# Performance work log

Measured on AMD Instinct MI355X. Metric: run time of the kernel, lower is better.

## Reference

```python
import jax, jax.numpy as jnp
import numpy as np
import math

B, D, H, W, C = 1, 16, 56, 56, 256
WD, WH, WW = 2, 7, 7
NH, NP = 8, 4
N = WD * WH * WW          # 98 tokens per window
HD = C // NH
NWIN = (D // WD) * (H // WH) * (W // WW)  # 512


def layernorm(x, g, b, eps=1e-5):
    m = x.mean(-1, keepdims=True)
    v = jnp.mean((x - m) ** 2, -1, keepdims=True)
    return (x - m) * jax.lax.rsqrt(v + eps) * g + b


def _reference_points():
    zz = (jnp.arange(WD, dtype=jnp.float32) + 0.5) / WD
    yy = (jnp.arange(WH, dtype=jnp.float32) + 0.5) / WH
    xx = (jnp.arange(WW, dtype=jnp.float32) + 0.5) / WW
    gz, gy, gx = jnp.meshgrid(zz, yy, xx, indexing='ij')
    return jnp.stack([gx.ravel(), gy.ravel(), gz.ravel()], -1)  # (N, 3) in xyz order


def _trilinear(value, loc):
    # value: (Bn, N, NH, HD); loc: (Bn, N, NH, NP, 3) normalized xyz in [0,1]
    # grid_sample semantics: align_corners=False, zero padding
    Bn = value.shape[0]
    v = value.transpose(0, 2, 1, 3)  # (Bn, NH, S, HD), S == N (window volume)
    px = loc[..., 0] * WW - 0.5
    py = loc[..., 1] * WH - 0.5
    pz = loc[..., 2] * WD - 0.5
    x0, y0, z0 = jnp.floor(px), jnp.floor(py), jnp.floor(pz)
    out = jnp.zeros(loc.shape[:-1] + (HD,), value.dtype)
    for dz in (0, 1):
        for dy in (0, 1):
            for dx in (0, 1):
                xi, yi, zi = x0 + dx, y0 + dy, z0 + dz
                wgt = (1 - jnp.abs(px - xi)) * (1 - jnp.abs(py - yi)) * (1 - jnp.abs(pz - zi))
                valid = ((xi >= 0) & (xi < WW) & (yi >= 0) & (yi < WH) & (zi >= 0) & (zi < WD)).astype(value.dtype)
                idx = (jnp.clip(zi, 0, WD - 1) * (WH * WW) + jnp.clip(yi, 0, WH - 1) * WW
                       + jnp.clip(xi, 0, WW - 1)).astype(jnp.int32)  # (Bn, N, NH, NP)
                idxf = idx.transpose(0, 2, 1, 3).reshape(Bn, NH, N * NP)
                g = jnp.take_along_axis(v, idxf[..., None], axis=2)  # (Bn, NH, N*NP, HD)
                g = g.reshape(Bn, NH, N, NP, HD).transpose(0, 2, 1, 3, 4)
                out = out + g * (wgt * valid)[..., None]
    return out  # (Bn, N, NH, NP, HD)


def setup_inputs():
    key = jax.random.key(0)
    ks = jax.random.split(key, 12)

    def lin(k, fin, fout):
        s = 1.0 / np.sqrt(fin)
        kw, kb = jax.random.split(k)
        return (jax.random.uniform(kw, (fin, fout), jnp.float32, -s, s),
                jax.random.uniform(kb, (fout,), jnp.float32, -s, s))

    val_w, val_b = lin(ks[2], C, C)
    off_w, off_b = lin(ks[3], C, NH * NP * 3)
    aw_w, aw_b = lin(ks[4], C, NH * NP)
    out_w, out_b = lin(ks[5], C, C)
    proj_w, proj_b = lin(ks[6], C, C)
    fc1_w, fc1_b = lin(ks[7], C, 4 * C)
    fc2_w, fc2_b = lin(ks[8], 4 * C, C)
    return dict(
        x=jax.random.normal(ks[0], (B, D, H, W, C), jnp.float32),
        mask=jax.random.uniform(ks[1], (NWIN, N, WD, WH, WW), jnp.float32),
        norm1_g=jnp.ones((C,), jnp.float32), norm1_b=jnp.zeros((C,), jnp.float32),
        val_w=val_w, val_b=val_b, off_w=off_w, off_b=off_b,
        aw_w=aw_w, aw_b=aw_b, out_w=out_w, out_b=out_b,
        anorm_g=jnp.ones((C,), jnp.float32), anorm_b=jnp.zeros((C,), jnp.float32),
        proj_w=proj_w, proj_b=proj_b,
        norm2_g=jnp.ones((C,), jnp.float32), norm2_b=jnp.zeros((C,), jnp.float32),
        fc1_w=fc1_w, fc1_b=fc1_b, fc2_w=fc2_w, fc2_b=fc2_b)


def reference(x, mask, norm1_g, norm1_b, val_w, val_b, off_w, off_b, aw_w, aw_b,
              out_w, out_b, anorm_g, anorm_b, proj_w, proj_b,
              norm2_g, norm2_b, fc1_w, fc1_b, fc2_w, fc2_b):
    shortcut = x
    xn = layernorm(x, norm1_g, norm1_b)
    # window partition (dims divisible by window, shift_size = 0 -> no pad/roll)
    xw = xn.reshape(B, D // WD, WD, H // WH, WH, W // WW, WW, C)
    xw = xw.transpose(0, 1, 3, 5, 2, 4, 6, 7).reshape(-1, N, C)  # (B*NWIN, N, C)
    Bn = B * NWIN
    # --- PositionEmbeddingSine over the per-window mask ---
    z_e = jnp.cumsum(mask, 2) * mask / math.pi
    y_e = jnp.cumsum(mask, 3) * mask / math.pi
    x_e = jnp.cumsum(mask, 4) * mask / math.pi
    emb = mask * (jnp.sin(x_e) + jnp.sin(math.pi * y_e) + z_e)
    emb = emb.reshape(NWIN, N, N)  # flatten(2); N == WD*WH*WW
    diag = jnp.diagonal(emb, axis1=1, axis2=2)  # (NWIN, N)
    q = (xw.reshape(B, NWIN, N, C) + diag[None, :, :, None]).reshape(Bn, N, C)
    # --- MS3DDeformAttn over single level = window ---
    ref = _reference_points()  # (N, 3)
    value = (xw @ val_w + val_b).reshape(Bn, N, NH, HD)
    off = (q @ off_w + off_b).reshape(Bn, N, NH, NP, 3)
    aw = jax.nn.softmax((q @ aw_w + aw_b).reshape(Bn, N, NH, NP), axis=-1)
    loc = ref[None, :, None, None, :] + off / jnp.array([WW, WH, WD], jnp.float32)
    sampled = _trilinear(value, loc)                       # (Bn, N, NH, NP, HD)
    attn = (sampled * aw[..., None]).sum(3).reshape(Bn, N, C) @ out_w + out_b
    # WindowAttention3D epilogue: proj(norm(x + attn))
    xw = layernorm(xw + attn, anorm_g, anorm_b) @ proj_w + proj_b
    # window reverse
    xr = xw.reshape(B, D // WD, H // WH, W // WW, WD, WH, WW, C)
    xr = xr.transpose(0, 1, 4, 2, 5, 3, 6, 7).reshape(B, D, H, W, C)
    x = shortcut + xr
    # MLP branch
    h = layernorm(x, norm2_g, norm2_b)
    h = jax.nn.gelu(h @ fc1_w + fc1_b)
    return x + (h @ fc2_w + fc2_b)
```

## Files before the change

### kernel.cpp

```cpp
#include <hip/hip_runtime.h>
#include <hip/hip_bf16.h>
#include <hip/hip_fp16.h>

#define B2F(x) __bfloat162float(x)
#define F2B(x) __float2bfloat16(x)

typedef __bf16 bf16x8 __attribute__((ext_vector_type(8)));
typedef float floatx4 __attribute__((ext_vector_type(4)));

static constexpr int MROWS = 50176;
static constexpr int CDIM  = 256;
static constexpr int MCHUNK = 25088;

enum { MODE_BF16 = 0, MODE_VALOFFAW = 1, MODE_REVERSE = 3, MODE_GELU = 4, MODE_FC2 = 5 };

#if defined(__has_builtin)
#if __has_builtin(__builtin_amdgcn_global_load_lds)
#define HAS_GLL 1
#endif
#endif
#ifndef HAS_GLL
#define HAS_GLL 0
#endif


__device__ __forceinline__ void win_decode(int r, int& tok) {
    int w = r / 98, n = r - w * 98;
    int dB = w >> 6, hB = (w >> 3) & 7, wB = w & 7;
    int z = n / 49, n2 = n - z * 49, yy = n2 / 7, xx = n2 - yy * 7;
    tok = ((dB * 2 + z) * 56 + hB * 7 + yy) * 56 + wB * 7 + xx;
}

__device__ __forceinline__ float bf2f(unsigned short u) {
    return __uint_as_float(((unsigned)u) << 16);
}

__device__ __forceinline__ float wave_sum64(float v) {
#pragma unroll
    for (int off = 32; off > 0; off >>= 1) v += __shfl_xor(v, off, 64);
    return v;
}


__global__ __launch_bounds__(256) void transpose_all(
    const float* __restrict__ val_w, const float* __restrict__ off_w,
    const float* __restrict__ aw_w,  const float* __restrict__ out_w,
    const float* __restrict__ proj_w, const float* __restrict__ fc1_w,
    const float* __restrict__ fc2_w,
    __hip_bfloat16* __restrict__ valT, __hip_bfloat16* __restrict__ offawT,
    __hip_bfloat16* __restrict__ outT, __hip_bfloat16* __restrict__ projT,
    __hip_bfloat16* __restrict__ fc1T, __hip_bfloat16* __restrict__ fc2T) {
    int bid = blockIdx.x;
    const float* src; __hip_bfloat16* dst; int K, N, base;
    if (bid < 256)       { src = val_w;  dst = valT;           K = 256;  N = 256;  base = 0; }
    else if (bid < 352)  { src = off_w;  dst = offawT;         K = 256;  N = 96;   base = 256; }
    else if (bid < 384)  { src = aw_w;   dst = offawT + 96*256; K = 256; N = 32;   base = 352; }
    else if (bid < 640)  { src = out_w;  dst = outT;           K = 256;  N = 256;  base = 384; }
    else if (bid < 896)  { src = proj_w; dst = projT;          K = 256;  N = 256;  base = 640; }
    else if (bid < 1920) { src = fc1_w;  dst = fc1T;           K = 256;  N = 1024; base = 896; }
    else                 { src = fc2_w;  dst = fc2T;           K = 1024; N = 256;  base = 1920; }
    int i = (bid - base) * 256 + threadIdx.x;
    if (i >= K * N) return;
    int nn = i / K, kk = i - nn * K;
    dst[(size_t)nn * K + kk] = F2B(src[(size_t)kk * N + nn]);
}


__global__ __launch_bounds__(256) void diag_colsum_kernel(
    const float* __restrict__ mask, float* __restrict__ diag,
    const __hip_bfloat16* __restrict__ wT, float* __restrict__ csum) {
    if (blockIdx.x == gridDim.x - 1) {
        int n = threadIdx.x;
        if (n < 128) {
            float s = 0.f;
            for (int k = 0; k < 256; ++k) s += B2F(wT[n * 256 + k]);
            csum[n] = s;
        }
        return;
    }
    int r = blockIdx.x * 256 + threadIdx.x;
    int n = r % 98;
    int z = n / 49, n2 = n - z * 49, yy = n2 / 7, xx = n2 - yy * 7;
    const float* mb = mask + (size_t)r * 98;
    float m = mb[z * 49 + yy * 7 + xx];
    float sz = 0.f, sy = 0.f, sx = 0.f;
    for (int k = 0; k <= z; ++k)  sz += mb[k * 49 + yy * 7 + xx];
    for (int k = 0; k <= yy; ++k) sy += mb[z * 49 + k * 7 + xx];
    for (int k = 0; k <= xx; ++k) sx += mb[z * 49 + yy * 7 + k];
    const float PI = 3.14159265358979323846f;
    diag[r] = m * (sinf(sx * m / PI) + sinf(sy * m) + sz * m / PI);
}


__global__ __launch_bounds__(256) void ln1_kernel(
    const float* __restrict__ x,
    const float* __restrict__ g, const float* __restrict__ b,
    __hip_bfloat16* __restrict__ xw) {
    const int lane = threadIdx.x & 63;
    const int r = blockIdx.x * 4 + (threadIdx.x >> 6);
    int tok; win_decode(r, tok);
    const int c0 = lane * 4;
    float4 v = *(const float4*)(x + (size_t)tok * CDIM + c0);
    float mean = wave_sum64(v.x + v.y + v.z + v.w) * (1.f / 256.f);
    float dx = v.x - mean, dy = v.y - mean, dz = v.z - mean, dw = v.w - mean;
    float var = wave_sum64(dx * dx + dy * dy + dz * dz + dw * dw) * (1.f / 256.f);
    float rstd = rsqrtf(var + 1e-5f);
    float4 gg = *(const float4*)(g + c0);
    float4 bb = *(const float4*)(b + c0);
    __hip_bfloat16 ob[4] = { F2B(dx * rstd * gg.x + bb.x), F2B(dy * rstd * gg.y + bb.y),
                             F2B(dz * rstd * gg.z + bb.z), F2B(dw * rstd * gg.w + bb.w) };
    *(ushort4*)(xw + (size_t)r * CDIM + c0) = *(const ushort4*)ob;
}

__global__ __launch_bounds__(256) void ln_a_kernel(
    const __hip_bfloat16* __restrict__ xw, const __hip_bfloat16* __restrict__ attn,
    const float* __restrict__ g, const float* __restrict__ b,
    __hip_bfloat16* a2) {
    const int lane = threadIdx.x & 63;
    const int r = blockIdx.x * 4 + (threadIdx.x >> 6);
    const int c0 = lane * 4;
    const size_t base = (size_t)r * CDIM + c0;
    ushort4 xv = *(const ushort4*)(xw + base);
    ushort4 av = *(const ushort4*)(attn + base);
    float tx = bf2f(xv.x) + bf2f(av.x);
    float ty = bf2f(xv.y) + bf2f(av.y);
    float tz = bf2f(xv.z) + bf2f(av.z);
    float tw = bf2f(xv.w) + bf2f(av.w);
    float mean = wave_sum64(tx + ty + tz + tw) * (1.f / 256.f);
    float dx = tx - mean, dy = ty - mean, dz = tz - mean, dw = tw - mean;
    float var = wave_sum64(dx * dx + dy * dy + dz * dz + dw * dw) * (1.f / 256.f);
    float rstd = rsqrtf(var + 1e-5f);
    float4 gg = *(const float4*)(g + c0);
    float4 bb = *(const float4*)(b + c0);
    __hip_bfloat16 ob[4] = { F2B(dx * rstd * gg.x + bb.x), F2B(dy * rstd * gg.y + bb.y),
                             F2B(dz * rstd * gg.z + bb.z), F2B(dw * rstd * gg.w + bb.w) };
    *(ushort4*)((__hip_bfloat16*)a2 + base) = *(const ushort4*)ob;
}

__global__ __launch_bounds__(256) void ln2_kernel(
    const float* __restrict__ xres,
    const float* __restrict__ g, const float* __restrict__ b,
    __hip_bfloat16* __restrict__ hin) {
    const int lane = threadIdx.x & 63;
    const int r = blockIdx.x * 4 + (threadIdx.x >> 6);
    const int c0 = lane * 4;
    float4 v = *(const float4*)(xres + (size_t)r * CDIM + c0);
    float mean = wave_sum64(v.x + v.y + v.z + v.w) * (1.f / 256.f);
    float dx = v.x - mean, dy = v.y - mean, dz = v.z - mean, dw = v.w - mean;
    float var = wave_sum64(dx * dx + dy * dy + dz * dz + dw * dw) * (1.f / 256.f);
    float rstd = rsqrtf(var + 1e-5f);
    float4 gg = *(const float4*)(g + c0);
    float4 bb = *(const float4*)(b + c0);
    __hip_bfloat16 ob[4] = { F2B(dx * rstd * gg.x + bb.x), F2B(dy * rstd * gg.y + bb.y),
                             F2B(dz * rstd * gg.z + bb.z), F2B(dw * rstd * gg.w + bb.w) };
    *(ushort4*)(hin + (size_t)r * CDIM + c0) = *(const ushort4*)ob;
}


__global__ __launch_bounds__(512, 6) void sample_fused(
    const __half* __restrict__ offaw,
    const __hip_bfloat16* __restrict__ value,
    __hip_bfloat16* __restrict__ ai) {
    __shared__ __align__(16) __hip_bfloat16 vs[98 * 256];
    const int tid = threadIdx.x;
    const int w = blockIdx.x;

    {
        const uint4* vsrc = (const uint4*)(value + (size_t)w * 98 * CDIM);
        uint4* vdst = (uint4*)vs;
        for (int i = tid; i < 98 * CDIM / 8; i += 512) vdst[i] = vsrc[i];
    }
    __syncthreads();

    const int lane  = tid & 63;
    const int wave  = tid >> 6;
    const int h     = lane >> 3;
    const int s     = lane & 7;
    const int p     = s >> 1;
    const int jbase = (s & 1) * 4;
    const int c0    = lane * 4;
    const int gbase = lane & ~7;

    for (int r = wave; r < 98; r += 8) {
        int z = r / 49, n2 = r - z * 49, yy = n2 / 7, xx = n2 - yy * 7;
        const __half* orow = offaw + ((size_t)w * 98 + r) * 128;

        float l0 = __half2float(orow[96 + h * 4 + 0]);
        float l1 = __half2float(orow[96 + h * 4 + 1]);
        float l2 = __half2float(orow[96 + h * 4 + 2]);
        float l3 = __half2float(orow[96 + h * 4 + 3]);
        float mx = fmaxf(fmaxf(l0, l1), fmaxf(l2, l3));
        float e0 = __expf(l0 - mx), e1 = __expf(l1 - mx), e2 = __expf(l2 - mx), e3 = __expf(l3 - mx);
        float inv = 1.f / (e0 + e1 + e2 + e3);
        float ep = (p == 0) ? e0 : (p == 1) ? e1 : (p == 2) ? e2 : e3;
        float wp = ep * inv;

        float ox = __half2float(orow[h * 12 + p * 3 + 0]);
        float oy = __half2float(orow[h * 12 + p * 3 + 1]);
        float oz = __half2float(orow[h * 12 + p * 3 + 2]);
        float px = (float)xx + ox, py = (float)yy + oy, pz = (float)z + oz;
        float fx0 = floorf(px), fy0 = floorf(py), fz0 = floorf(pz);
        int ix = (int)fx0, iy = (int)fy0, iz = (int)fz0;
        float fx = px - fx0, fy = py - fy0, fz = pz - fz0;

        uint packed[4];
#pragma unroll
        for (int jj = 0; jj < 4; ++jj) {
            int j = jbase + jj;
            int dzz = j >> 2, dyy = (j >> 1) & 1, dxx = j & 1;
            int zi = iz + dzz, yi = iy + dyy, xi = ix + dxx;
            float wz = dzz ? fz : 1.f - fz;
            float wy = dyy ? fy : 1.f - fy;
            float wxw = dxx ? fx : 1.f - fx;
            bool valid = (zi >= 0) & (zi < 2) & (yi >= 0) & (yi < 7) & (xi >= 0) & (xi < 7);
            float wc = valid ? wp * wz * wy * wxw : 0.f;
            int zc = min(max(zi, 0), 1), yc = min(max(yi, 0), 6), xc = min(max(xi, 0), 6);
            int idx = zc * 49 + yc * 7 + xc;
            packed[jj] = ((uint)idx << 16) | (uint)__half_as_ushort(__float2half(wc));
        }

        float a0 = 0.f, a1 = 0.f, a2 = 0.f, a3 = 0.f;
#pragma unroll
        for (int jj = 0; jj < 4; ++jj) {
            uint mine = packed[jj];
#pragma unroll
            for (int sl = 0; sl < 8; ++sl) {
                uint pk = __shfl(mine, gbase + sl, 64);
                float wj = __half2float(__ushort_as_half((unsigned short)(pk & 0xffffu)));
                int idx = (int)(pk >> 16);
                ushort4 v = *(const ushort4*)(vs + (size_t)idx * CDIM + c0);
                a0 += wj * bf2f(v.x);
                a1 += wj * bf2f(v.y);
                a2 += wj * bf2f(v.z);
                a3 += wj * bf2f(v.w);
            }
        }
        __hip_bfloat16 ob[4] = { F2B(a0), F2B(a1), F2B(a2), F2B(a3) };
        *(ushort4*)(ai + ((size_t)w * 98 + r) * CDIM + c0) = *(const ushort4*)ob;
    }
}


template <int MODE>
__global__ __launch_bounds__(256) void gemm_bt(
    const __hip_bfloat16* __restrict__ A,
    const __hip_bfloat16* __restrict__ Bt,
    const int N, const int K,
    const float* __restrict__ bias0,
    const float* __restrict__ bias1,
    const float* __restrict__ bias2,
    void* C,
    void* extra,
    const void* extra2,
    const float* __restrict__ csum) {
    __shared__ __align__(16) __hip_bfloat16 As[2][128 * 32];
    __shared__ __align__(16) __hip_bfloat16 Bs[2][128 * 32];
    const int tid  = threadIdx.x;
    const int lane = tid & 63;
    const int wave = tid >> 6;
    const int wm = (wave >> 1) * 64;
    const int wn = (wave & 1) * 64;
    const int row0 = blockIdx.x * 128;
    const int col0 = blockIdx.y * 128;
    const int l15 = lane & 15;
    const int quad = lane >> 4;

    floatx4 acc[4][4] = {};

    const int sr = tid >> 2;
    const int sk = (tid & 3) * 8;

    const __hip_bfloat16* Ab = A + (size_t)row0 * K + sr * (size_t)K + sk;
    const __hip_bfloat16* Bb = Bt + (size_t)col0 * K + sr * (size_t)K + sk;
    const size_t half64 = (size_t)64 * K;

    auto stage = [&](int buf, int k0) {
#if HAS_GLL
        __builtin_amdgcn_global_load_lds(
            (const __attribute__((address_space(1))) void*)(Ab + k0),
            (__attribute__((address_space(3))) void*)(&As[buf][sr * 32 + sk]), 16, 0, 0);
        __builtin_amdgcn_global_load_lds(
            (const __attribute__((address_space(1))) void*)(Ab + half64 + k0),
            (__attribute__((address_space(3))) void*)(&As[buf][(sr + 64) * 32 + sk]), 16, 0, 0);
        __builtin_amdgcn_global_load_lds(
            (const __attribute__((address_space(1))) void*)(Bb + k0),
            (__attribute__((address_space(3))) void*)(&Bs[buf][sr * 32 + sk]), 16, 0, 0);
        __builtin_amdgcn_global_load_lds(
            (const __attribute__((address_space(1))) void*)(Bb + half64 + k0),
            (__attribute__((address_space(3))) void*)(&Bs[buf][(sr + 64) * 32 + sk]), 16, 0, 0);
#else
        *reinterpret_cast<uint4*>(&As[buf][sr * 32 + sk]) = *reinterpret_cast<const uint4*>(Ab + k0);
        *reinterpret_cast<uint4*>(&As[buf][(sr + 64) * 32 + sk]) = *reinterpret_cast<const uint4*>(Ab + half64 + k0);
        *reinterpret_cast<uint4*>(&Bs[buf][sr * 32 + sk]) = *reinterpret_cast<const uint4*>(Bb + k0);
        *reinterpret_cast<uint4*>(&Bs[buf][(sr + 64) * 32 + sk]) = *reinterpret_cast<const uint4*>(Bb + half64 + k0);
#endif
    };

    const int nk = K >> 5;
    stage(0, 0);
    for (int t = 0; t < nk; ++t) {
        __syncthreads();
        if (t + 1 < nk) stage((t + 1) & 1, (t + 1) * 32);
        const __hip_bfloat16* Asb = As[t & 1];
        const __hip_bfloat16* Bsb = Bs[t & 1];
        bf16x8 af[4], bfg[4];
#pragma unroll
        for (int i = 0; i < 4; ++i)
            af[i] = *reinterpret_cast<const bf16x8*>(&Asb[(wm + i * 16 + l15) * 32 + quad * 8]);
#pragma unroll
        for (int j = 0; j < 4; ++j)
            bfg[j] = *reinterpret_cast<const bf16x8*>(&Bsb[(wn + j * 16 + l15) * 32 + quad * 8]);
#pragma unroll
        for (int i = 0; i < 4; ++i)
#pragma unroll
            for (int j = 0; j < 4; ++j)
                acc[i][j] = __builtin_amdgcn_mfma_f32_16x16x32_bf16(af[i], bfg[j], acc[i][j], 0, 0, 0);
    }

#pragma unroll
    for (int i = 0; i < 4; ++i) {
#pragma unroll
        for (int j = 0; j < 4; ++j) {
#pragma unroll
            for (int rr = 0; rr < 4; ++rr) {
                int row = row0 + wm + i * 16 + quad * 4 + rr;
                int col = col0 + wn + j * 16 + l15;
                float v = acc[i][j][rr];
                if constexpr (MODE == MODE_BF16) {
                    v += bias0[col];
                    ((__hip_bfloat16*)C)[(size_t)row * N + col] = F2B(v);
                } else if constexpr (MODE == MODE_VALOFFAW) {
                    if (col < 256) {
                        v += bias0[col];
                        ((__hip_bfloat16*)C)[(size_t)row * 256 + col] = F2B(v);
                    } else {
                        int c2 = col - 256;
                        const float* diag = (const float*)extra2;
                        v += (c2 < 96 ? bias1[c2] : bias2[c2 - 96]);
                        v += diag[row] * csum[c2];
                        ((__half*)extra)[(size_t)row * 128 + c2] = __float2half(v);
                    }
                } else if constexpr (MODE == MODE_REVERSE) {
                    v += bias0[col];
                    int tok; win_decode(row, tok);
                    const float* xin = (const float*)extra2;
                    ((float*)C)[(size_t)tok * CDIM + col] = xin[(size_t)tok * CDIM + col] + v;
                } else if constexpr (MODE == MODE_GELU) {
                    v += bias0[col];
                    float t2 = 1.5957691216057308f * (v + 0.044715f * v * v * v);
                    v = v / (1.f + __expf(-t2));
                    ((__hip_bfloat16*)C)[(size_t)row * N + col] = F2B(v);
                } else {
                    v += bias0[col];
                    const float* xres = (const float*)extra2;
                    v += xres[(size_t)row * CDIM + col];
                    ((float*)C)[(size_t)row * CDIM + col] = v;
                }
            }
        }
    }
}


extern "C" void kernel_launch(void* const* d_in, const int* in_sizes, int n_in,
                              void* d_out, int out_size, void* d_ws, size_t ws_size,
                              hipStream_t stream) {
    const float* x      = (const float*)d_in[0];
    const float* mask   = (const float*)d_in[1];
    const float* n1g    = (const float*)d_in[2];
    const float* n1b    = (const float*)d_in[3];
    const float* val_w  = (const float*)d_in[4];
    const float* val_b  = (const float*)d_in[5];
    const float* off_w  = (const float*)d_in[6];
    const float* off_b  = (const float*)d_in[7];
    const float* aw_w   = (const float*)d_in[8];
    const float* aw_b   = (const float*)d_in[9];
    const float* out_w  = (const float*)d_in[10];
    const float* out_b  = (const float*)d_in[11];
    const float* ang    = (const float*)d_in[12];
    const float* anb    = (const float*)d_in[13];
    const float* proj_w = (const float*)d_in[14];
    const float* proj_b = (const float*)d_in[15];
    const float* n2g    = (const float*)d_in[16];
    const float* n2b    = (const float*)d_in[17];
    const float* fc1_w  = (const float*)d_in[18];
    const float* fc1_b  = (const float*)d_in[19];
    const float* fc2_w  = (const float*)d_in[20];
    const float* fc2_b  = (const float*)d_in[21];

    char* ws = (char*)d_ws;
    size_t o = 0;
    auto alloc = [&](size_t bytes) {
        size_t r = o;
        o += (bytes + 255) & ~(size_t)255;
        return r;
    };
    const size_t M = MROWS;
    const size_t REGION_B = M * 128 * 2 + M * 256 * 2 + M * 256 * 2;

    __hip_bfloat16* valT    = (__hip_bfloat16*)(ws + alloc(256 * 256 * 2));
    __hip_bfloat16* offawT  = (__hip_bfloat16*)(ws + alloc(128 * 256 * 2));
    __hip_bfloat16* outT    = (__hip_bfloat16*)(ws + alloc(256 * 256 * 2));
    __hip_bfloat16* projT   = (__hip_bfloat16*)(ws + alloc(256 * 256 * 2));
    __hip_bfloat16* fc1T    = (__hip_bfloat16*)(ws + alloc(1024 * 256 * 2));
    __hip_bfloat16* fc2T    = (__hip_bfloat16*)(ws + alloc(256 * 1024 * 2));
    float*          csum    = (float*)(ws + alloc(128 * 4));
    float*          diag    = (float*)(ws + alloc(M * 4));
    char*           slab1   = ws + alloc(M * 256 * 2);
    char*           region  = ws + alloc(REGION_B);
    (void)ws_size; (void)in_sizes; (void)n_in; (void)out_size;

    __hip_bfloat16* xw    = (__hip_bfloat16*)slab1;
    __hip_bfloat16* a2    = (__hip_bfloat16*)slab1;
    __hip_bfloat16* hin   = (__hip_bfloat16*)slab1;
    __half*         offaw = (__half*)region;
    __hip_bfloat16* ai    = (__hip_bfloat16*)(region + M * 128 * 2);
    __hip_bfloat16* hbuf  = (__hip_bfloat16*)region;
    __hip_bfloat16* value = (__hip_bfloat16*)d_out;
    __hip_bfloat16* attn  = (__hip_bfloat16*)d_out;
    float*          xres  = (float*)d_out;

    dim3 blk(256);
    hipLaunchKernelGGL(transpose_all, dim3(2944), blk, 0, stream,
                       val_w, off_w, aw_w, out_w, proj_w, fc1_w, fc2_w,
                       valT, offawT, outT, projT, fc1T, fc2T);
    hipLaunchKernelGGL(diag_colsum_kernel, dim3(MROWS / 256 + 1), blk, 0, stream,
                       mask, diag, offawT, csum);

    hipLaunchKernelGGL(ln1_kernel, dim3(MROWS / 4), blk, 0, stream, x, n1g, n1b, xw);
    hipLaunchKernelGGL((gemm_bt<MODE_VALOFFAW>), dim3(MROWS / 128, 3), blk, 0, stream,
                       xw, valT, 384, 256, val_b, off_b, aw_b,
                       (void*)value, (void*)offaw, (const void*)diag, csum);
    hipLaunchKernelGGL(sample_fused, dim3(MROWS / 98), dim3(512), 0, stream,
                       offaw, value, ai);
    hipLaunchKernelGGL((gemm_bt<MODE_BF16>), dim3(MROWS / 128, 2), blk, 0, stream,
                       ai, outT, 256, 256, out_b, (const float*)nullptr, (const float*)nullptr,
                       (void*)attn, (void*)nullptr, (const void*)nullptr, (const float*)nullptr);
    hipLaunchKernelGGL(ln_a_kernel, dim3(MROWS / 4), blk, 0, stream, xw, attn, ang, anb, a2);
    hipLaunchKernelGGL((gemm_bt<MODE_REVERSE>), dim3(MROWS / 128, 2), blk, 0, stream,
                       a2, projT, 256, 256, proj_b, (const float*)nullptr, (const float*)nullptr,
                       (void*)xres, (void*)nullptr, (const void*)x, (const float*)nullptr);
    hipLaunchKernelGGL(ln2_kernel, dim3(MROWS / 4), blk, 0, stream, xres, n2g, n2b, hin);
    for (int c = 0; c < 2; ++c) {
        const __hip_bfloat16* hin_c = hin + (size_t)c * MCHUNK * 256;
        float*                out_c = (float*)d_out + (size_t)c * MCHUNK * 256;
        hipLaunchKernelGGL((gemm_bt<MODE_GELU>), dim3(MCHUNK / 128, 8), blk, 0, stream,
                           hin_c, fc1T, 1024, 256, fc1_b, (const float*)nullptr, (const float*)nullptr,
                           (void*)hbuf, (void*)nullptr, (const void*)nullptr, (const float*)nullptr);
        hipLaunchKernelGGL((gemm_bt<MODE_FC2>), dim3(MCHUNK / 128, 2), blk, 0, stream,
                           hbuf, fc2T, 256, 1024, fc2_b, (const float*)nullptr, (const float*)nullptr,
                           (void*)out_c, (void*)nullptr, (const void*)out_c, (const float*)nullptr);
    }
}
```

Before: 514.5 us.

## Fuse prologue kernels, stage offsets in LDS, fold residual into out-proj GEMM

Merges the weight transpose, diag/colsum and LN1 kernels into one launch, and computes the column sums from the fp32 weights. The sampling kernel now stages the offset/attention rows in LDS alongside the values, using global_load_lds when available, and packs byte offsets so the inner gather skips an index multiply. The out-proj GEMM adds the xw residual in its epilogue, so the LN kernel reads one tensor instead of two. The MLP runs as a single chunk when the workspace is large enough. The trade-off is extra LDS per block, which lowers the occupancy hint for the sampling kernel.

```diff
diff --git a/kernel.cpp b/kernel.cpp
--- a/kernel.cpp
+++ b/kernel.cpp
@@ -12,7 +12,7 @@
 static constexpr int CDIM  = 256;
 static constexpr int MCHUNK = 25088;
 
-enum { MODE_BF16 = 0, MODE_VALOFFAW = 1, MODE_REVERSE = 3, MODE_GELU = 4, MODE_FC2 = 5 };
+enum { MODE_BF16 = 0, MODE_VALOFFAW = 1, MODE_REVERSE = 3, MODE_GELU = 4, MODE_FC2 = 5, MODE_ATTN = 6 };
 
 #if defined(__has_builtin)
 #if __has_builtin(__builtin_amdgcn_global_load_lds)
@@ -42,7 +42,10 @@
 }
 
 
-__global__ __launch_bounds__(256) void transpose_all(
+__global__ __launch_bounds__(256) void fused_pre(
+    const float* __restrict__ x, const float* __restrict__ n1g, const float* __restrict__ n1b,
+    __hip_bfloat16* __restrict__ xw,
+    const float* __restrict__ mask, float* __restrict__ diag, float* __restrict__ csum,
     const float* __restrict__ val_w, const float* __restrict__ off_w,
     const float* __restrict__ aw_w,  const float* __restrict__ out_w,
     const float* __restrict__ proj_w, const float* __restrict__ fc1_w,
@@ -50,82 +53,74 @@
     __hip_bfloat16* __restrict__ valT, __hip_bfloat16* __restrict__ offawT,
     __hip_bfloat16* __restrict__ outT, __hip_bfloat16* __restrict__ projT,
     __hip_bfloat16* __restrict__ fc1T, __hip_bfloat16* __restrict__ fc2T) {
-    int bid = blockIdx.x;
-    const float* src; __hip_bfloat16* dst; int K, N, base;
-    if (bid < 256)       { src = val_w;  dst = valT;           K = 256;  N = 256;  base = 0; }
-    else if (bid < 352)  { src = off_w;  dst = offawT;         K = 256;  N = 96;   base = 256; }
-    else if (bid < 384)  { src = aw_w;   dst = offawT + 96*256; K = 256; N = 32;   base = 352; }
-    else if (bid < 640)  { src = out_w;  dst = outT;           K = 256;  N = 256;  base = 384; }
-    else if (bid < 896)  { src = proj_w; dst = projT;          K = 256;  N = 256;  base = 640; }
-    else if (bid < 1920) { src = fc1_w;  dst = fc1T;           K = 256;  N = 1024; base = 896; }
-    else                 { src = fc2_w;  dst = fc2T;           K = 1024; N = 256;  base = 1920; }
-    int i = (bid - base) * 256 + threadIdx.x;
-    if (i >= K * N) return;
-    int nn = i / K, kk = i - nn * K;
-    dst[(size_t)nn * K + kk] = F2B(src[(size_t)kk * N + nn]);
-}
-
-
-__global__ __launch_bounds__(256) void diag_colsum_kernel(
-    const float* __restrict__ mask, float* __restrict__ diag,
-    const __hip_bfloat16* __restrict__ wT, float* __restrict__ csum) {
-    if (blockIdx.x == gridDim.x - 1) {
-        int n = threadIdx.x;
-        if (n < 128) {
+    const int bid = blockIdx.x;
+    const int tid = threadIdx.x;
+
+    if (bid < 2944) {
+        const float* src; __hip_bfloat16* dst; int K, N, base;
+        if (bid < 256)       { src = val_w;  dst = valT;            K = 256;  N = 256;  base = 0; }
+        else if (bid < 352)  { src = off_w;  dst = offawT;          K = 256;  N = 96;   base = 256; }
+        else if (bid < 384)  { src = aw_w;   dst = offawT + 96*256; K = 256;  N = 32;   base = 352; }
+        else if (bid < 640)  { src = out_w;  dst = outT;            K = 256;  N = 256;  base = 384; }
+        else if (bid < 896)  { src = proj_w; dst = projT;           K = 256;  N = 256;  base = 640; }
+        else if (bid < 1920) { src = fc1_w;  dst = fc1T;            K = 256;  N = 1024; base = 896; }
+        else                 { src = fc2_w;  dst = fc2T;            K = 1024; N = 256;  base = 1920; }
+        int i = (bid - base) * 256 + tid;
+        if (i >= K * N) return;
+        int nn = i / K, kk = i - nn * K;
+        dst[(size_t)nn * K + kk] = F2B(src[(size_t)kk * N + nn]);
+    } else if (bid < 3140) {
+        int r = (bid - 2944) * 256 + tid;
+        int n = r % 98;
+        int z = n / 49, n2 = n - z * 49, yy = n2 / 7, xx = n2 - yy * 7;
+        const float* mb = mask + (size_t)r * 98;
+        float m = mb[z * 49 + yy * 7 + xx];
+        float sz = 0.f, sy = 0.f, sx = 0.f;
+        for (int k = 0; k <= z; ++k)  sz += mb[k * 49 + yy * 7 + xx];
+        for (int k = 0; k <= yy; ++k) sy += mb[z * 49 + k * 7 + xx];
+        for (int k = 0; k <= xx; ++k) sx += mb[z * 49 + yy * 7 + k];
+        const float PI = 3.14159265358979323846f;
+        diag[r] = m * (sinf(sx * m / PI) + sinf(sy * m) + sz * m / PI);
+    } else if (bid == 3140) {
+        if (tid < 96) {
             float s = 0.f;
-            for (int k = 0; k < 256; ++k) s += B2F(wT[n * 256 + k]);
-            csum[n] = s;
-        }
-        return;
-    }
-    int r = blockIdx.x * 256 + threadIdx.x;
-    int n = r % 98;
-    int z = n / 49, n2 = n - z * 49, yy = n2 / 7, xx = n2 - yy * 7;
-    const float* mb = mask + (size_t)r * 98;
-    float m = mb[z * 49 + yy * 7 + xx];
-    float sz = 0.f, sy = 0.f, sx = 0.f;
-    for (int k = 0; k <= z; ++k)  sz += mb[k * 49 + yy * 7 + xx];
-    for (int k = 0; k <= yy; ++k) sy += mb[z * 49 + k * 7 + xx];
-    for (int k = 0; k <= xx; ++k) sx += mb[z * 49 + yy * 7 + k];
-    const float PI = 3.14159265358979323846f;
-    diag[r] = m * (sinf(sx * m / PI) + sinf(sy * m) + sz * m / PI);
-}
-
-
-__global__ __launch_bounds__(256) void ln1_kernel(
-    const float* __restrict__ x,
-    const float* __restrict__ g, const float* __restrict__ b,
-    __hip_bfloat16* __restrict__ xw) {
-    const int lane = threadIdx.x & 63;
-    const int r = blockIdx.x * 4 + (threadIdx.x >> 6);
-    int tok; win_decode(r, tok);
-    const int c0 = lane * 4;
-    float4 v = *(const float4*)(x + (size_t)tok * CDIM + c0);
-    float mean = wave_sum64(v.x + v.y + v.z + v.w) * (1.f / 256.f);
-    float dx = v.x - mean, dy = v.y - mean, dz = v.z - mean, dw = v.w - mean;
-    float var = wave_sum64(dx * dx + dy * dy + dz * dz + dw * dw) * (1.f / 256.f);
-    float rstd = rsqrtf(var + 1e-5f);
-    float4 gg = *(const float4*)(g + c0);
-    float4 bb = *(const float4*)(b + c0);
-    __hip_bfloat16 ob[4] = { F2B(dx * rstd * gg.x + bb.x), F2B(dy * rstd * gg.y + bb.y),
-                             F2B(dz * rstd * gg.z + bb.z), F2B(dw * rstd * gg.w + bb.w) };
-    *(ushort4*)(xw + (size_t)r * CDIM + c0) = *(const ushort4*)ob;
-}
+            for (int k = 0; k < 256; ++k) s += off_w[(size_t)k * 96 + tid];
+            csum[tid] = s;
+        } else if (tid < 128) {
+            int n = tid - 96;
+            float s = 0.f;
+            for (int k = 0; k < 256; ++k) s += aw_w[(size_t)k * 32 + n];
+            csum[tid] = s;
+        }
+    } else {
+        const int lane = tid & 63;
+        const int r = (bid - 3141) * 4 + (tid >> 6);
+        int tok; win_decode(r, tok);
+        const int c0 = lane * 4;
+        float4 v = *(const float4*)(x + (size_t)tok * CDIM + c0);
+        float mean = wave_sum64(v.x + v.y + v.z + v.w) * (1.f / 256.f);
+        float dx = v.x - mean, dy = v.y - mean, dz = v.z - mean, dw = v.w - mean;
+        float var = wave_sum64(dx * dx + dy * dy + dz * dz + dw * dw) * (1.f / 256.f);
+        float rstd = rsqrtf(var + 1e-5f);
+        float4 gg = *(const float4*)(n1g + c0);
+        float4 bb = *(const float4*)(n1b + c0);
+        __hip_bfloat16 ob[4] = { F2B(dx * rstd * gg.x + bb.x), F2B(dy * rstd * gg.y + bb.y),
+                                 F2B(dz * rstd * gg.z + bb.z), F2B(dw * rstd * gg.w + bb.w) };
+        *(ushort4*)(xw + (size_t)r * CDIM + c0) = *(const ushort4*)ob;
+    }
+}
+
 
 __global__ __launch_bounds__(256) void ln_a_kernel(
-    const __hip_bfloat16* __restrict__ xw, const __hip_bfloat16* __restrict__ attn,
+    const __hip_bfloat16* __restrict__ s,
     const float* __restrict__ g, const float* __restrict__ b,
     __hip_bfloat16* a2) {
     const int lane = threadIdx.x & 63;
     const int r = blockIdx.x * 4 + (threadIdx.x >> 6);
     const int c0 = lane * 4;
     const size_t base = (size_t)r * CDIM + c0;
-    ushort4 xv = *(const ushort4*)(xw + base);
-    ushort4 av = *(const ushort4*)(attn + base);
-    float tx = bf2f(xv.x) + bf2f(av.x);
-    float ty = bf2f(xv.y) + bf2f(av.y);
-    float tz = bf2f(xv.z) + bf2f(av.z);
-    float tw = bf2f(xv.w) + bf2f(av.w);
+    ushort4 sv = *(const ushort4*)(s + base);
+    float tx = bf2f(sv.x), ty = bf2f(sv.y), tz = bf2f(sv.z), tw = bf2f(sv.w);
     float mean = wave_sum64(tx + ty + tz + tw) * (1.f / 256.f);
     float dx = tx - mean, dy = ty - mean, dz = tz - mean, dw = tw - mean;
     float var = wave_sum64(dx * dx + dy * dy + dz * dz + dw * dw) * (1.f / 256.f);
@@ -157,19 +152,46 @@
 }
 
 
-__global__ __launch_bounds__(512, 6) void sample_fused(
+__global__ __launch_bounds__(512, 4) void sample_fused(
     const __half* __restrict__ offaw,
     const __hip_bfloat16* __restrict__ value,
     __hip_bfloat16* __restrict__ ai) {
     __shared__ __align__(16) __hip_bfloat16 vs[98 * 256];
+    __shared__ __align__(16) __half os[98 * 128];
     const int tid = threadIdx.x;
     const int w = blockIdx.x;
 
+#if HAS_GLL
+    {
+        const uint4* vsrc = (const uint4*)(value + (size_t)w * 98 * CDIM);
+#pragma unroll
+        for (int k = 0; k < 7; ++k) {
+            int i = tid + k * 512;
+            if (i < 3136)
+                __builtin_amdgcn_global_load_lds(
+                    (const __attribute__((address_space(1))) void*)(vsrc + i),
+                    (__attribute__((address_space(3))) void*)(((uint4*)vs) + i), 16, 0, 0);
+        }
+        const uint4* osrc = (const uint4*)(offaw + (size_t)w * 98 * 128);
+#pragma unroll
+        for (int k = 0; k < 4; ++k) {
+            int i = tid + k * 512;
+            if (i < 1568)
+                __builtin_amdgcn_global_load_lds(
+                    (const __attribute__((address_space(1))) void*)(osrc + i),
+                    (__attribute__((address_space(3))) void*)(((uint4*)os) + i), 16, 0, 0);
+        }
+    }
+#else
     {
         const uint4* vsrc = (const uint4*)(value + (size_t)w * 98 * CDIM);
         uint4* vdst = (uint4*)vs;
-        for (int i = tid; i < 98 * CDIM / 8; i += 512) vdst[i] = vsrc[i];
-    }
+        for (int i = tid; i < 3136; i += 512) vdst[i] = vsrc[i];
+        const uint4* osrc = (const uint4*)(offaw + (size_t)w * 98 * 128);
+        uint4* odst = (uint4*)os;
+        for (int i = tid; i < 1568; i += 512) odst[i] = osrc[i];
+    }
+#endif
     __syncthreads();
 
     const int lane  = tid & 63;
@@ -178,12 +200,12 @@
     const int s     = lane & 7;
     const int p     = s >> 1;
     const int jbase = (s & 1) * 4;
-    const int c0    = lane * 4;
+    const int boff  = lane * 8;
     const int gbase = lane & ~7;
 
     for (int r = wave; r < 98; r += 8) {
         int z = r / 49, n2 = r - z * 49, yy = n2 / 7, xx = n2 - yy * 7;
-        const __half* orow = offaw + ((size_t)w * 98 + r) * 128;
+        const __half* orow = os + r * 128;
 
         float l0 = __half2float(orow[96 + h * 4 + 0]);
         float l1 = __half2float(orow[96 + h * 4 + 1]);
@@ -216,7 +238,7 @@
             float wc = valid ? wp * wz * wy * wxw : 0.f;
             int zc = min(max(zi, 0), 1), yc = min(max(yi, 0), 6), xc = min(max(xi, 0), 6);
             int idx = zc * 49 + yc * 7 + xc;
-            packed[jj] = ((uint)idx << 16) | (uint)__half_as_ushort(__float2half(wc));
+            packed[jj] = ((uint)(idx * 512) << 16) | (uint)__half_as_ushort(__float2half(wc));
         }
 
         float a0 = 0.f, a1 = 0.f, a2 = 0.f, a3 = 0.f;
@@ -227,8 +249,7 @@
             for (int sl = 0; sl < 8; ++sl) {
                 uint pk = __shfl(mine, gbase + sl, 64);
                 float wj = __half2float(__ushort_as_half((unsigned short)(pk & 0xffffu)));
-                int idx = (int)(pk >> 16);
-                ushort4 v = *(const ushort4*)(vs + (size_t)idx * CDIM + c0);
+                ushort4 v = *(const ushort4*)((const char*)vs + (pk >> 16) + boff);
                 a0 += wj * bf2f(v.x);
                 a1 += wj * bf2f(v.y);
                 a2 += wj * bf2f(v.z);
@@ -236,7 +257,7 @@
             }
         }
         __hip_bfloat16 ob[4] = { F2B(a0), F2B(a1), F2B(a2), F2B(a3) };
-        *(ushort4*)(ai + ((size_t)w * 98 + r) * CDIM + c0) = *(const ushort4*)ob;
+        *(ushort4*)(ai + ((size_t)w * 98 + r) * CDIM + lane * 4) = *(const ushort4*)ob;
     }
 }
 
@@ -328,6 +349,11 @@
                 float v = acc[i][j][rr];
                 if constexpr (MODE == MODE_BF16) {
                     v += bias0[col];
+                    ((__hip_bfloat16*)C)[(size_t)row * N + col] = F2B(v);
+                } else if constexpr (MODE == MODE_ATTN) {
+                    v += bias0[col];
+                    const __hip_bfloat16* xwp = (const __hip_bfloat16*)extra2;
+                    v += B2F(xwp[(size_t)row * 256 + col]);
                     ((__hip_bfloat16*)C)[(size_t)row * N + col] = F2B(v);
                 } else if constexpr (MODE == MODE_VALOFFAW) {
                     if (col < 256) {
@@ -396,7 +422,6 @@
         return r;
     };
     const size_t M = MROWS;
-    const size_t REGION_B = M * 128 * 2 + M * 256 * 2 + M * 256 * 2;
 
     __hip_bfloat16* valT    = (__hip_bfloat16*)(ws + alloc(256 * 256 * 2));
     __hip_bfloat16* offawT  = (__hip_bfloat16*)(ws + alloc(128 * 256 * 2));
@@ -407,8 +432,13 @@
     float*          csum    = (float*)(ws + alloc(128 * 4));
     float*          diag    = (float*)(ws + alloc(M * 4));
     char*           slab1   = ws + alloc(M * 256 * 2);
-    char*           region  = ws + alloc(REGION_B);
-    (void)ws_size; (void)in_sizes; (void)n_in; (void)out_size;
+    char*           region  = ws + o;
+    size_t          avail   = (ws_size > o) ? (ws_size - o) : 0;
+    (void)in_sizes; (void)n_in; (void)out_size;
+
+    const bool  full = avail >= (size_t)M * 1024 * 2 + 256;
+    const int   nch  = full ? 1 : 2;
+    const int   MC   = full ? MROWS : MCHUNK;
 
     __hip_bfloat16* xw    = (__hip_bfloat16*)slab1;
     __hip_bfloat16* a2    = (__hip_bfloat16*)slab1;
@@ -421,33 +451,30 @@
     float*          xres  = (float*)d_out;
 
     dim3 blk(256);
-    hipLaunchKernelGGL(transpose_all, dim3(2944), blk, 0, stream,
+    hipLaunchKernelGGL(fused_pre, dim3(2944 + 196 + 1 + MROWS / 4), blk, 0, stream,
+                       x, n1g, n1b, xw, mask, diag, csum,
                        val_w, off_w, aw_w, out_w, proj_w, fc1_w, fc2_w,
                        valT, offawT, outT, projT, fc1T, fc2T);
-    hipLaunchKernelGGL(diag_colsum_kernel, dim3(MROWS / 256 + 1), blk, 0, stream,
-                       mask, diag, offawT, csum);
-
-    hipLaunchKernelGGL(ln1_kernel, dim3(MROWS / 4), blk, 0, stream, x, n1g, n1b, xw);
     hipLaunchKernelGGL((gemm_bt<MODE_VALOFFAW>), dim3(MROWS / 128, 3), blk, 0, stream,
                        xw, valT, 384, 256, val_b, off_b, aw_b,
                        (void*)value, (void*)offaw, (const void*)diag, csum);
     hipLaunchKernelGGL(sample_fused, dim3(MROWS / 98), dim3(512), 0, stream,
                        offaw, value, ai);
-    hipLaunchKernelGGL((gemm_bt<MODE_BF16>), dim3(MROWS / 128, 2), blk, 0, stream,
+    hipLaunchKernelGGL((gemm_bt<MODE_ATTN>), dim3(MROWS / 128, 2), blk, 0, stream,
                        ai, outT, 256, 256, out_b, (const float*)nullptr, (const float*)nullptr,
-                       (void*)attn, (void*)nullptr, (const void*)nullptr, (const float*)nullptr);
-    hipLaunchKernelGGL(ln_a_kernel, dim3(MROWS / 4), blk, 0, stream, xw, attn, ang, anb, a2);
+                       (void*)attn, (void*)nullptr, (const void*)xw, (const float*)nullptr);
+    hipLaunchKernelGGL(ln_a_kernel, dim3(MROWS / 4), blk, 0, stream, attn, ang, anb, a2);
     hipLaunchKernelGGL((gemm_bt<MODE_REVERSE>), dim3(MROWS / 128, 2), blk, 0, stream,
                        a2, projT, 256, 256, proj_b, (const float*)nullptr, (const float*)nullptr,
                        (void*)xres, (void*)nullptr, (const void*)x, (const float*)nullptr);
     hipLaunchKernelGGL(ln2_kernel, dim3(MROWS / 4), blk, 0, stream, xres, n2g, n2b, hin);
-    for (int c = 0; c < 2; ++c) {
-        const __hip_bfloat16* hin_c = hin + (size_t)c * MCHUNK * 256;
-        float*                out_c = (float*)d_out + (size_t)c * MCHUNK * 256;
-        hipLaunchKernelGGL((gemm_bt<MODE_GELU>), dim3(MCHUNK / 128, 8), blk, 0, stream,
+    for (int c = 0; c < nch; ++c) {
+        const __hip_bfloat16* hin_c = hin + (size_t)c * MC * 256;
+        float*                out_c = (float*)d_out + (size_t)c * MC * 256;
+        hipLaunchKernelGGL((gemm_bt<MODE_GELU>), dim3(MC / 128, 8), blk, 0, stream,
                            hin_c, fc1T, 1024, 256, fc1_b, (const float*)nullptr, (const float*)nullptr,
                            (void*)hbuf, (void*)nullptr, (const void*)nullptr, (const float*)nullptr);
-        hipLaunchKernelGGL((gemm_bt<MODE_FC2>), dim3(MCHUNK / 128, 2), blk, 0, stream,
+        hipLaunchKernelGGL((gemm_bt<MODE_FC2>), dim3(MC / 128, 2), blk, 0, stream,
                            hbuf, fc2T, 256, 1024, fc2_b, (const float*)nullptr, (const float*)nullptr,
                            (void*)out_c, (void*)nullptr, (const void*)out_c, (const float*)nullptr);
     }
```

New measurement: 500.2 us. 1.03x faster.
